# Kernel optimization log

Hardware: AMD Instinct MI355X
Metric: run time of the kernel (lower is better)

Reference implementation:

```python
import jax, jax.numpy as jnp
import numpy as np

H = 64  # hidden size

def _lstm_last_h(x, W_ih, W_hh, b_ih, b_hh):
    # x: [B, T]; PyTorch LSTM gate order: i, f, g, o (each H wide in 4H axis)
    B, T = x.shape
    # input_size == 1, so x @ W_ih.T == x[..., None] * W_ih[:, 0]
    xproj = x[:, :, None] * W_ih[:, 0][None, None, :] + (b_ih + b_hh)  # [B, T, 4H]
    xproj_t = jnp.swapaxes(xproj, 0, 1)  # [T, B, 4H] for scan over time

    def step(carry, xp_t):
        h, c = carry
        gates = xp_t + h @ W_hh.T  # [B, 4H]
        i = jax.nn.sigmoid(gates[:, 0 * H:1 * H])
        f = jax.nn.sigmoid(gates[:, 1 * H:2 * H])
        g = jnp.tanh(gates[:, 2 * H:3 * H])
        o = jax.nn.sigmoid(gates[:, 3 * H:4 * H])
        c = f * c + i * g
        h = o * jnp.tanh(c)
        return (h, c), None

    h0 = jnp.zeros((B, H), x.dtype)
    c0 = jnp.zeros((B, H), x.dtype)
    (h_last, _), _ = jax.lax.scan(step, (h0, c0), xproj_t)
    return h_last  # [B, H] == lstm_out[:, -1, :]


def setup_inputs() -> dict:
    key = jax.random.key(0)
    ks = jax.random.split(key, 7)
    B, T = 2048, 512
    s_ih = 1.0 / np.sqrt(H)
    return {
        "x": jax.random.normal(ks[0], (B, T), jnp.float32),
        "W_ih": jax.random.uniform(ks[1], (4 * H, 1), jnp.float32, -s_ih, s_ih),
        "W_hh": jax.random.uniform(ks[2], (4 * H, H), jnp.float32, -s_ih, s_ih),
        "b_ih": jax.random.uniform(ks[3], (4 * H,), jnp.float32, -s_ih, s_ih),
        "b_hh": jax.random.uniform(ks[4], (4 * H,), jnp.float32, -s_ih, s_ih),
        "W_d": jax.random.uniform(ks[5], (1, H), jnp.float32, -s_ih, s_ih),
        "b_d": jax.random.uniform(ks[6], (1,), jnp.float32, -s_ih, s_ih),
    }


def reference(x, W_ih, W_hh, b_ih, b_hh, W_d, b_d):
    h_last = _lstm_last_h(x, W_ih, W_hh, b_ih, b_hh)  # [B, H]
    out = h_last @ W_d.T + b_d  # [B, 1]
    return out[:, 0]  # squeeze(1) -> [B]
```

## Files before the change

kernel.cpp:

```cpp
#include <hip/hip_runtime.h>

#define TLEN 512
#define HID  64

typedef _Float16 half8 __attribute__((ext_vector_type(8)));
typedef float    f32x4 __attribute__((ext_vector_type(4)));

__device__ __forceinline__ float rcp_fast(float x) { return __builtin_amdgcn_rcpf(x); }
__device__ __forceinline__ float exp2_fast(float x) {
#if __has_builtin(__builtin_amdgcn_exp2f)
    return __builtin_amdgcn_exp2f(x);
#else
    float r; asm("v_exp_f32 %0, %1" : "=v"(r) : "v"(x)); return r;
#endif
}

__global__ __launch_bounds__(256) __attribute__((amdgpu_waves_per_eu(2, 2)))
void lstm_r18(const float* __restrict__ x,
              const float* __restrict__ W_ih,
              const float* __restrict__ W_hh,
              const float* __restrict__ b_ih,
              const float* __restrict__ b_hh,
              const float* __restrict__ W_d,
              const float* __restrict__ b_d,
              float* __restrict__ out) {
    __shared__ __align__(16) float    xs[4][516];
    __shared__ __align__(16) _Float16 hbuf[2][4][80];

    const int tid = threadIdx.x;
    const int L   = tid & 63;
    const int w   = tid >> 6;
    const int r0  = blockIdx.x * 4;

    for (int i = tid; i < 4 * 128; i += 256) {
        const int r = i >> 7, t4 = (i & 127) * 4;
        *(float4*)&xs[r][t4] = *(const float4*)&x[(size_t)(r0 + r) * TLEN + t4];
    }
    for (int i = tid; i < 2 * 4 * 80; i += 256)
        ((_Float16*)hbuf)[i] = (_Float16)0.0f;

    const float K  = 1.44269504f;
    const float K2 = 2.0f * K;

    half8 af[4][2];
    {
        const int m  = L & 15;
        const int g  = m & 3;
        const int kb = (L >> 4) * 8;
        const float sg = (g == 2) ? K2 : -K;
#pragma unroll
        for (int tt = 0; tt < 4; ++tt) {
            const int uu = 16 * w + 4 * tt + (m >> 2);
            const float* row = &W_hh[(size_t)(g * HID + uu) * HID];
#pragma unroll
            for (int q = 0; q < 2; ++q) {
                const float* p = row + 32 * q + kb;
                half8 hf;
#pragma unroll
                for (int i = 0; i < 8; ++i) hf[i] = (_Float16)(sg * p[i]);
                af[tt][q] = hf;
            }
        }
    }

    const int c   = L & 15;
    const int b   = c & 3;
    const int dup = c >> 2;
    const int u   = 16 * w + 4 * dup + (L >> 4);
    const bool d1 = dup & 1;
    const bool d2 = dup & 2;

    float wih[4], bias[4];
#pragma unroll
    for (int g = 0; g < 4; ++g) {
        const float s = (g == 2) ? K2 : -K;
        wih[g]  = s * W_ih[g * HID + u];
        bias[g] = s * (b_ih[g * HID + u] + b_hh[g * HID + u]);
    }

    const float* xrow = &xs[b][0];
    const int koff = (L >> 4) * 8;
    const _Float16* h0r = &hbuf[0][b][0];
    _Float16*       h0w = &hbuf[0][0][0];
    const _Float16* h1r = &hbuf[1][b][0];
    _Float16*       h1w = &hbuf[1][0][0];
    const int widx = b * 80 + u;
    const f32x4 zero = {0.0f, 0.0f, 0.0f, 0.0f};
    float S = 0.0f;

    __syncthreads();

    auto step = [&](const _Float16* hin, _Float16* hout, float xt) {
        const float pre0 = fmaf(xt, wih[0], bias[0]);
        const float pre1 = fmaf(xt, wih[1], bias[1]);
        const float pre2 = fmaf(xt, wih[2], bias[2]);
        const float pre3 = fmaf(xt, wih[3], bias[3]);

        half8 b0 = *(const half8*)(hin + koff);
        half8 b1 = *(const half8*)(hin + koff + 32);

        f32x4 t0 = __builtin_amdgcn_mfma_f32_16x16x32_f16(af[0][0], b0, zero, 0, 0, 0);
        f32x4 t1 = __builtin_amdgcn_mfma_f32_16x16x32_f16(af[1][0], b0, zero, 0, 0, 0);
        f32x4 t2 = __builtin_amdgcn_mfma_f32_16x16x32_f16(af[2][0], b0, zero, 0, 0, 0);
        f32x4 t3 = __builtin_amdgcn_mfma_f32_16x16x32_f16(af[3][0], b0, zero, 0, 0, 0);
        t0 = __builtin_amdgcn_mfma_f32_16x16x32_f16(af[0][1], b1, t0, 0, 0, 0);
        t1 = __builtin_amdgcn_mfma_f32_16x16x32_f16(af[1][1], b1, t1, 0, 0, 0);
        t2 = __builtin_amdgcn_mfma_f32_16x16x32_f16(af[2][1], b1, t2, 0, 0, 0);
        t3 = __builtin_amdgcn_mfma_f32_16x16x32_f16(af[3][1], b1, t3, 0, 0, 0);

        f32x4 dS;
#pragma unroll
        for (int r = 0; r < 4; ++r) {
            const float a01 = d1 ? t1[r] : t0[r];
            const float a23 = d1 ? t3[r] : t2[r];
            dS[r] = d2 ? a23 : a01;
        }

        const float ei = exp2_fast(dS[0] + pre0);
        const float ef = exp2_fast(dS[1] + pre1);
        const float eg = exp2_fast(dS[2] + pre2);
        const float eo = exp2_fast(dS[3] + pre3);

        const float A1  = 1.0f + ei;
        const float B1  = 1.0f + eg;
        const float E1  = 1.0f + ef;
        const float C1K = fmaf(eg, K2, -K2);
        const float Pig = A1 * B1;
        const float Dde = E1 * Pig;
        const float CEK = C1K * E1;
        const float num = fmaf(S, Pig, CEK);
        S = num * rcp_fast(Dde);
        const float ec = exp2_fast(S);
        const float F1 = 1.0f + eo;
        const float G1 = 1.0f + ec;
        const float H1 = ec - 1.0f;
        const float hv = H1 * rcp_fast(F1 * G1);
        hout[widx] = (_Float16)hv;
    };

    for (int t = 0; t < TLEN; t += 4) {
        const float4 xq = *(const float4*)&xrow[t];
        step(h0r, h1w, xq.x);
        __syncthreads();
        step(h1r, h0w, xq.y);
        __syncthreads();
        step(h0r, h1w, xq.z);
        __syncthreads();
        step(h1r, h0w, xq.w);
        __syncthreads();
    }

    float pv = (float)hbuf[0][w][L] * W_d[L];
#pragma unroll
    for (int off = 32; off > 0; off >>= 1)
        pv += __shfl_xor(pv, off, 64);
    if (L == 0)
        out[r0 + w] = pv + b_d[0];
}

extern "C" void kernel_launch(void* const* d_in, const int* in_sizes, int n_in,
                              void* d_out, int out_size, void* d_ws, size_t ws_size,
                              hipStream_t stream) {
    const float* x    = (const float*)d_in[0];
    const float* W_ih = (const float*)d_in[1];
    const float* W_hh = (const float*)d_in[2];
    const float* b_ih = (const float*)d_in[3];
    const float* b_hh = (const float*)d_in[4];
    const float* W_d  = (const float*)d_in[5];
    const float* b_d  = (const float*)d_in[6];
    float* out = (float*)d_out;

    dim3 grid(512);
    dim3 block(256);
    lstm_r18<<<grid, block, 0, stream>>>(x, W_ih, W_hh, b_ih, b_hh, W_d, b_d, out);
}
```

Before: 206.5 us.

## Ping-pong two LSTM batch groups so MFMA and cell math overlap

Each block now handles 8 rows split into two 4-row groups, each owned by four waves. The halves alternate: while one group's waves run the recurrent MFMA, the other group's waves run the gate and cell math. The aim is to overlap matrix-core latency with the transcendental ALU work. In exchange the grid is halved to 256 blocks of 512 threads, and each phase still requires a block-wide barrier, so two barriers per timestep are shared across both groups.

After: 276.5 us. +33.9%, slower.

```diff
diff --git a/kernel.cpp b/kernel.cpp
--- a/kernel.cpp
+++ b/kernel.cpp
@@ -15,29 +15,32 @@
 #endif
 }
 
-__global__ __launch_bounds__(256) __attribute__((amdgpu_waves_per_eu(2, 2)))
-void lstm_r18(const float* __restrict__ x,
-              const float* __restrict__ W_ih,
-              const float* __restrict__ W_hh,
-              const float* __restrict__ b_ih,
-              const float* __restrict__ b_hh,
-              const float* __restrict__ W_d,
-              const float* __restrict__ b_d,
-              float* __restrict__ out) {
-    __shared__ __align__(16) float    xs[4][516];
-    __shared__ __align__(16) _Float16 hbuf[2][4][80];
+__global__ __launch_bounds__(512) __attribute__((amdgpu_waves_per_eu(2, 2)))
+void lstm_pipe(const float* __restrict__ x,
+               const float* __restrict__ W_ih,
+               const float* __restrict__ W_hh,
+               const float* __restrict__ b_ih,
+               const float* __restrict__ b_hh,
+               const float* __restrict__ W_d,
+               const float* __restrict__ b_d,
+               float* __restrict__ out) {
+    __shared__ __align__(16) float    xs[8][516];
+    __shared__ __align__(16) _Float16 hb[2][4][80];
 
     const int tid = threadIdx.x;
     const int L   = tid & 63;
     const int w   = tid >> 6;
-    const int r0  = blockIdx.x * 4;
+    const int isA = (w < 4) ? 1 : 0;
+    const int wl  = w & 3;
+    const int gi  = 1 - isA;
+    const int r0  = blockIdx.x * 8;
 
-    for (int i = tid; i < 4 * 128; i += 256) {
+    for (int i = tid; i < 8 * 128; i += 512) {
         const int r = i >> 7, t4 = (i & 127) * 4;
         *(float4*)&xs[r][t4] = *(const float4*)&x[(size_t)(r0 + r) * TLEN + t4];
     }
-    for (int i = tid; i < 2 * 4 * 80; i += 256)
-        ((_Float16*)hbuf)[i] = (_Float16)0.0f;
+    for (int i = tid; i < 2 * 4 * 80; i += 512)
+        ((_Float16*)hb)[i] = (_Float16)0.0f;
 
     const float K  = 1.44269504f;
     const float K2 = 2.0f * K;
@@ -50,7 +53,7 @@
         const float sg = (g == 2) ? K2 : -K;
 #pragma unroll
         for (int tt = 0; tt < 4; ++tt) {
-            const int uu = 16 * w + 4 * tt + (m >> 2);
+            const int uu = 16 * wl + 4 * tt + (m >> 2);
             const float* row = &W_hh[(size_t)(g * HID + uu) * HID];
 #pragma unroll
             for (int q = 0; q < 2; ++q) {
@@ -66,7 +69,7 @@
     const int c   = L & 15;
     const int b   = c & 3;
     const int dup = c >> 2;
-    const int u   = 16 * w + 4 * dup + (L >> 4);
+    const int u   = 16 * wl + 4 * dup + (L >> 4);
     const bool d1 = dup & 1;
     const bool d2 = dup & 2;
 
@@ -78,36 +81,33 @@
         bias[g] = s * (b_ih[g * HID + u] + b_hh[g * HID + u]);
     }
 
-    const float* xrow = &xs[b][0];
+    const float* xrow = &xs[gi * 4 + b][0];
     const int koff = (L >> 4) * 8;
-    const _Float16* h0r = &hbuf[0][b][0];
-    _Float16*       h0w = &hbuf[0][0][0];
-    const _Float16* h1r = &hbuf[1][b][0];
-    _Float16*       h1w = &hbuf[1][0][0];
+    const _Float16* hrd = &hb[gi][b][0];
+    _Float16*       hwr = &hb[gi][0][0];
     const int widx = b * 80 + u;
     const f32x4 zero = {0.0f, 0.0f, 0.0f, 0.0f};
+
+    f32x4 t0, t1, t2, t3;
     float S = 0.0f;
 
     __syncthreads();
 
-    auto step = [&](const _Float16* hin, _Float16* hout, float xt) {
-        const float pre0 = fmaf(xt, wih[0], bias[0]);
-        const float pre1 = fmaf(xt, wih[1], bias[1]);
-        const float pre2 = fmaf(xt, wih[2], bias[2]);
-        const float pre3 = fmaf(xt, wih[3], bias[3]);
-
-        half8 b0 = *(const half8*)(hin + koff);
-        half8 b1 = *(const half8*)(hin + koff + 32);
-
-        f32x4 t0 = __builtin_amdgcn_mfma_f32_16x16x32_f16(af[0][0], b0, zero, 0, 0, 0);
-        f32x4 t1 = __builtin_amdgcn_mfma_f32_16x16x32_f16(af[1][0], b0, zero, 0, 0, 0);
-        f32x4 t2 = __builtin_amdgcn_mfma_f32_16x16x32_f16(af[2][0], b0, zero, 0, 0, 0);
-        f32x4 t3 = __builtin_amdgcn_mfma_f32_16x16x32_f16(af[3][0], b0, zero, 0, 0, 0);
+    auto mfma_phase = [&]() {
+        const half8 b0 = *(const half8*)(hrd + koff);
+        const half8 b1 = *(const half8*)(hrd + koff + 32);
+        t0 = __builtin_amdgcn_mfma_f32_16x16x32_f16(af[0][0], b0, zero, 0, 0, 0);
+        t1 = __builtin_amdgcn_mfma_f32_16x16x32_f16(af[1][0], b0, zero, 0, 0, 0);
+        t2 = __builtin_amdgcn_mfma_f32_16x16x32_f16(af[2][0], b0, zero, 0, 0, 0);
+        t3 = __builtin_amdgcn_mfma_f32_16x16x32_f16(af[3][0], b0, zero, 0, 0, 0);
         t0 = __builtin_amdgcn_mfma_f32_16x16x32_f16(af[0][1], b1, t0, 0, 0, 0);
         t1 = __builtin_amdgcn_mfma_f32_16x16x32_f16(af[1][1], b1, t1, 0, 0, 0);
         t2 = __builtin_amdgcn_mfma_f32_16x16x32_f16(af[2][1], b1, t2, 0, 0, 0);
         t3 = __builtin_amdgcn_mfma_f32_16x16x32_f16(af[3][1], b1, t3, 0, 0, 0);
+    };
 
+    auto cell_phase = [&](int k) {
+        const float xt = xrow[k];
         f32x4 dS;
 #pragma unroll
         for (int r = 0; r < 4; ++r) {
@@ -115,12 +115,10 @@
             const float a23 = d1 ? t3[r] : t2[r];
             dS[r] = d2 ? a23 : a01;
         }
-
-        const float ei = exp2_fast(dS[0] + pre0);
-        const float ef = exp2_fast(dS[1] + pre1);
-        const float eg = exp2_fast(dS[2] + pre2);
-        const float eo = exp2_fast(dS[3] + pre3);
-
+        const float ei = exp2_fast(fmaf(xt, wih[0], bias[0]) + dS[0]);
+        const float ef = exp2_fast(fmaf(xt, wih[1], bias[1]) + dS[1]);
+        const float eg = exp2_fast(fmaf(xt, wih[2], bias[2]) + dS[2]);
+        const float eo = exp2_fast(fmaf(xt, wih[3], bias[3]) + dS[3]);
         const float A1  = 1.0f + ei;
         const float B1  = 1.0f + eg;
         const float E1  = 1.0f + ef;
@@ -135,22 +133,23 @@
         const float G1 = 1.0f + ec;
         const float H1 = ec - 1.0f;
         const float hv = H1 * rcp_fast(F1 * G1);
-        hout[widx] = (_Float16)hv;
+        hwr[widx] = (_Float16)hv;
     };
 
-    for (int t = 0; t < TLEN; t += 4) {
-        const float4 xq = *(const float4*)&xrow[t];
-        step(h0r, h1w, xq.x);
+    if (isA) mfma_phase();
+    __syncthreads();
+    for (int k = 0; k < TLEN - 1; ++k) {
+        if (isA) cell_phase(k); else mfma_phase();
         __syncthreads();
-        step(h1r, h0w, xq.y);
-        __syncthreads();
-        step(h0r, h1w, xq.z);
-        __syncthreads();
-        step(h1r, h0w, xq.w);
+        if (isA) mfma_phase(); else cell_phase(k);
         __syncthreads();
     }
+    if (isA) cell_phase(TLEN - 1); else mfma_phase();
+    __syncthreads();
+    if (!isA) cell_phase(TLEN - 1);
+    __syncthreads();
 
-    float pv = (float)hbuf[0][w][L] * W_d[L];
+    float pv = (float)hb[w >> 2][w & 3][L] * W_d[L];
 #pragma unroll
     for (int off = 32; off > 0; off >>= 1)
         pv += __shfl_xor(pv, off, 64);
@@ -170,7 +169,7 @@
     const float* b_d  = (const float*)d_in[6];
     float* out = (float*)d_out;
 
-    dim3 grid(512);
-    dim3 block(256);
-    lstm_r18<<<grid, block, 0, stream>>>(x, W_ih, W_hh, b_ih, b_hh, W_d, b_d, out);
+    dim3 grid(256);
+    dim3 block(512);
+    lstm_pipe<<<grid, block, 0, stream>>>(x, W_ih, W_hh, b_ih, b_hh, W_d, b_d, out);
 }
```
